# Optimization experiments

Hardware: AMD Instinct MI355X
Metric: run time of the kernel (lower is better)

The kernel has to match this reference:

```python
import jax, jax.numpy as jnp
import numpy as np


def setup_inputs() -> dict:
    key = jax.random.key(0)
    k1, k2 = jax.random.split(key)
    N, M, Q, D = 4096, 128, 64, 128
    a_embeddings = jax.random.normal(k1, (N, D), dtype=jnp.float32)
    b_embedding_sets = jax.random.normal(k2, (M, Q, D), dtype=jnp.float32)
    gaussian_variance = jnp.full((1,), 0.5, dtype=jnp.float32)  # nn.Parameter default
    return {
        "a_embeddings": a_embeddings,
        "b_embedding_sets": b_embedding_sets,
        "gaussian_variance": gaussian_variance,
    }


def reference(a_embeddings, b_embedding_sets, gaussian_variance):
    # Covariance = var * I, so inv(cov) = I / var and the Mahalanobis term is
    # ||a - mu||^2 / var. Expand the squared distance to avoid the NxMxQxD
    # broadcast intermediate the torch code materializes (same math).
    inv_var = 1.0 / gaussian_variance[0]
    a2 = jnp.sum(a_embeddings * a_embeddings, axis=-1)          # [N]
    b2 = jnp.sum(b_embedding_sets * b_embedding_sets, axis=-1)  # [M, Q]
    ab = jnp.einsum("nd,mqd->nmq", a_embeddings, b_embedding_sets)  # [N, M, Q]
    x2 = (a2[:, None, None] - 2.0 * ab + b2[None, :, :]) * inv_var  # [N, M, Q]
    densities = jnp.exp(-0.5 * x2)                  # [N, M, Q]
    dens_per_cluster = densities.sum(axis=2)        # [N, M]
    prob = dens_per_cluster / (dens_per_cluster.sum(axis=1, keepdims=True) + 1e-10)
    return prob
```

## Files before the change

kernel.cpp:

```cpp
#include <hip/hip_runtime.h>
#include <hip/hip_bf16.h>
#include <math.h>

#define NN 4096
#define MM 128
#define QQ 64
#define DD 128
#define CC (MM * QQ)

typedef short bf16x8 __attribute__((ext_vector_type(8)));
typedef float f32x4  __attribute__((ext_vector_type(4)));

static __device__ inline unsigned short f2bf(float f) {
    __hip_bfloat16 h = __float2bfloat16(f);
    return *reinterpret_cast<unsigned short*>(&h);
}

__global__ __launch_bounds__(256)
void prep_kernel(const float* __restrict__ A, const float* __restrict__ B,
                 unsigned short* __restrict__ Abf, unsigned short* __restrict__ Bbf,
                 float* __restrict__ a2, float* __restrict__ b2)
{
    const int row = blockIdx.x * 8 + (threadIdx.x >> 5);
    const int l32 = threadIdx.x & 31;
    const float* src;
    unsigned short* dst;
    float* nrm;
    if (row < NN) { src = A + (size_t)row * DD; dst = Abf + (size_t)row * DD; nrm = a2 + row; }
    else {
        int r = row - NN;
        src = B + (size_t)r * DD; dst = Bbf + (size_t)r * DD; nrm = b2 + r;
    }
    float4 v = ((const float4*)src)[l32];
    ushort4 u;
    u.x = f2bf(v.x); u.y = f2bf(v.y); u.z = f2bf(v.z); u.w = f2bf(v.w);
    ((ushort4*)dst)[l32] = u;
    float s = v.x * v.x + v.y * v.y + v.z * v.z + v.w * v.w;
    #pragma unroll
    for (int m = 16; m > 0; m >>= 1) s += __shfl_xor(s, m, 64);
    if (l32 == 0) *nrm = s;
}

__global__ __launch_bounds__(512, 4)
void kde_mfma_kernel(const unsigned short* __restrict__ Abf,
                     const unsigned short* __restrict__ Bbf,
                     const float* __restrict__ var,
                     const float* __restrict__ a2w,
                     const float* __restrict__ b2w,
                     float* __restrict__ dpc)
{
    __shared__ unsigned short Tile[256 * DD];
    __shared__ float a2s[128];
    __shared__ float b2s[128];
    __shared__ float red[8][32];

    const int lin = blockIdx.x;
    const int xcd = lin & 7;
    const int loc = lin >> 3;
    const int cb  = (xcd << 3) | (loc & 7);
    const int nb  = loc >> 3;
    const int n0  = nb * 128;
    const int c0  = cb * 128;

    const int t    = threadIdx.x;
    const int w    = t >> 6;
    const int lane = t & 63;

    const unsigned short* Ab = Abf + (size_t)n0 * DD;
    const unsigned short* Bb = Bbf + (size_t)c0 * DD;
    #pragma unroll
    for (int i = 0; i < 8; ++i) {
        const int slot = w * 512 + i * 64 + lane;
        const int r    = slot >> 4;
        const int c16  = slot & 15;
        const int scb  = c16 ^ (r & 7);
        const unsigned short* g = (r < 128) ? (Ab + r * DD + scb * 8)
                                            : (Bb + (r - 128) * DD + scb * 8);
        unsigned short* lbase = &Tile[(w * 512 + i * 64) * 8];
        __builtin_amdgcn_global_load_lds(
            (const __attribute__((address_space(1))) unsigned int*)g,
            (__attribute__((address_space(3))) unsigned int*)lbase,
            16, 0, 0);
    }
    if (t < 128)            a2s[t]       = a2w[n0 + t];
    else if (t < 256)       b2s[t - 128] = b2w[c0 + (t - 128)];
    __syncthreads();

    const int l15   = lane & 15;
    const int q     = lane >> 4;
    const int xr    = l15 & 7;
    const int rbase = (w & 3) * 32;
    const int cbase = (w >> 2) * 64;

    f32x4 acc[2][4] = {};
    #pragma unroll
    for (int ks = 0; ks < 4; ++ks) {
        const int off = ((ks * 4 + q) ^ xr) * 8;
        bf16x8 af[2], bf[4];
        #pragma unroll
        for (int i = 0; i < 2; ++i)
            af[i] = *(const bf16x8*)&Tile[(rbase + i * 16 + l15) * DD + off];
        #pragma unroll
        for (int j = 0; j < 4; ++j)
            bf[j] = *(const bf16x8*)&Tile[(128 + cbase + j * 16 + l15) * DD + off];
        #pragma unroll
        for (int i = 0; i < 2; ++i)
            #pragma unroll
            for (int j = 0; j < 4; ++j)
                acc[i][j] = __builtin_amdgcn_mfma_f32_16x16x32_bf16(
                                af[i], bf[j], acc[i][j], 0, 0, 0);
    }

    const float hinv = 0.5f / var[0];
    float rowsum[2][4];
    #pragma unroll
    for (int i = 0; i < 2; ++i) {
        #pragma unroll
        for (int reg = 0; reg < 4; ++reg) {
            const float a2 = a2s[rbase + i * 16 + q * 4 + reg];
            float p = 0.f;
            #pragma unroll
            for (int j = 0; j < 4; ++j) {
                const float b2 = b2s[cbase + j * 16 + l15];
                p += __expf((2.f * acc[i][j][reg] - a2 - b2) * hinv);
            }
            rowsum[i][reg] = p;
        }
    }
    #pragma unroll
    for (int mask = 1; mask < 16; mask <<= 1)
        #pragma unroll
        for (int i = 0; i < 2; ++i)
            #pragma unroll
            for (int reg = 0; reg < 4; ++reg)
                rowsum[i][reg] += __shfl_xor(rowsum[i][reg], mask, 64);

    if (l15 == 0) {
        #pragma unroll
        for (int i = 0; i < 2; ++i)
            #pragma unroll
            for (int reg = 0; reg < 4; ++reg)
                red[w][i * 16 + q * 4 + reg] = rowsum[i][reg];
    }
    const int m = (cb << 1) + (w >> 2);
    if (lane < 32)
        dpc[(size_t)m * NN + n0 + rbase + lane] = red[w][lane];
}

__global__ __launch_bounds__(1024)
void kde_norm_kernel(const float* __restrict__ dpc, float* __restrict__ out)
{
    __shared__ float tile[MM][65];
    __shared__ float rden[64];
    const int n0 = blockIdx.x * 64;
    const int t  = threadIdx.x;

    #pragma unroll
    for (int it = 0; it < 2; ++it) {
        const int m  = (t >> 4) + it * 64;
        const int nc = (t & 15) * 4;
        float4 v = *(const float4*)&dpc[(size_t)m * NN + n0 + nc];
        tile[m][nc]     = v.x;
        tile[m][nc + 1] = v.y;
        tile[m][nc + 2] = v.z;
        tile[m][nc + 3] = v.w;
    }
    __syncthreads();

    if (t < 64) {
        float s = 0.f;
        #pragma unroll 8
        for (int m = 0; m < MM; ++m) s += tile[m][t];
        rden[t] = 1.f / (s + 1e-10f);
    }
    __syncthreads();

    const int nloc = t >> 4;
    const int m0   = (t & 15) * 8;
    const float r  = rden[nloc];
    float4 o0, o1;
    o0.x = tile[m0][nloc] * r;     o0.y = tile[m0 + 1][nloc] * r;
    o0.z = tile[m0 + 2][nloc] * r; o0.w = tile[m0 + 3][nloc] * r;
    o1.x = tile[m0 + 4][nloc] * r; o1.y = tile[m0 + 5][nloc] * r;
    o1.z = tile[m0 + 6][nloc] * r; o1.w = tile[m0 + 7][nloc] * r;
    float* obase = &out[(size_t)(n0 + nloc) * MM + m0];
    *(float4*)obase       = o0;
    *(float4*)(obase + 4) = o1;
}

extern "C" void kernel_launch(void* const* d_in, const int* in_sizes, int n_in,
                              void* d_out, int out_size, void* d_ws, size_t ws_size,
                              hipStream_t stream) {
    const float* A   = (const float*)d_in[0];
    const float* B   = (const float*)d_in[1];
    const float* var = (const float*)d_in[2];
    float* out = (float*)d_out;

    unsigned short* Abf = (unsigned short*)d_ws;
    unsigned short* Bbf = Abf + (size_t)NN * DD;
    float* a2  = (float*)(Bbf + (size_t)CC * DD);
    float* b2  = a2 + NN;
    float* dpc = b2 + CC;

    prep_kernel<<<(NN + CC) / 8, 256, 0, stream>>>(A, B, Abf, Bbf, a2, b2);
    kde_mfma_kernel<<<2048, 512, 0, stream>>>(Abf, Bbf, var, a2, b2, dpc);
    kde_norm_kernel<<<NN / 64, 1024, 0, stream>>>(dpc, out);
}
```

Baseline: 85.90 us.

## Make density kernel persistent over center tiles with double-buffered B loads

Replaces the one-tile-per-block density kernel with 256 blocks that keep a 128-row A tile resident in LDS and iterate over eight 128-center B tiles. The B tiles and their norms are double-buffered via async global-to-LDS loads, so the next tile streams in while the current one is processed. This removes repeated A reloads and per-block launch and setup cost, and stores row sums directly as vectors. The trade-off is lower parallelism: one 8-wave block per CU, with hand-written waitcnt/barrier synchronisation.

```diff
diff --git a/kernel.cpp b/kernel.cpp
--- a/kernel.cpp
+++ b/kernel.cpp
@@ -10,6 +10,9 @@
 
 typedef short bf16x8 __attribute__((ext_vector_type(8)));
 typedef float f32x4  __attribute__((ext_vector_type(4)));
+
+#define AS1 __attribute__((address_space(1)))
+#define AS3 __attribute__((address_space(3)))
 
 static __device__ inline unsigned short f2bf(float f) {
     __hip_bfloat16 h = __float2bfloat16(f);
@@ -41,110 +44,132 @@
     if (l32 == 0) *nrm = s;
 }
 
-__global__ __launch_bounds__(512, 4)
-void kde_mfma_kernel(const unsigned short* __restrict__ Abf,
+__global__ __launch_bounds__(512, 2)
+void kde_dens_kernel(const unsigned short* __restrict__ Abf,
                      const unsigned short* __restrict__ Bbf,
                      const float* __restrict__ var,
                      const float* __restrict__ a2w,
                      const float* __restrict__ b2w,
                      float* __restrict__ dpc)
 {
-    __shared__ unsigned short Tile[256 * DD];
-    __shared__ float a2s[128];
-    __shared__ float b2s[128];
-    __shared__ float red[8][32];
-
-    const int lin = blockIdx.x;
-    const int xcd = lin & 7;
-    const int loc = lin >> 3;
-    const int cb  = (xcd << 3) | (loc & 7);
-    const int nb  = loc >> 3;
-    const int n0  = nb * 128;
-    const int c0  = cb * 128;
-
-    const int t    = threadIdx.x;
-    const int w    = t >> 6;
-    const int lane = t & 63;
-
-    const unsigned short* Ab = Abf + (size_t)n0 * DD;
-    const unsigned short* Bb = Bbf + (size_t)c0 * DD;
-    #pragma unroll
-    for (int i = 0; i < 8; ++i) {
-        const int slot = w * 512 + i * 64 + lane;
-        const int r    = slot >> 4;
-        const int c16  = slot & 15;
-        const int scb  = c16 ^ (r & 7);
-        const unsigned short* g = (r < 128) ? (Ab + r * DD + scb * 8)
-                                            : (Bb + (r - 128) * DD + scb * 8);
-        unsigned short* lbase = &Tile[(w * 512 + i * 64) * 8];
-        __builtin_amdgcn_global_load_lds(
-            (const __attribute__((address_space(1))) unsigned int*)g,
-            (__attribute__((address_space(3))) unsigned int*)lbase,
-            16, 0, 0);
-    }
-    if (t < 128)            a2s[t]       = a2w[n0 + t];
-    else if (t < 256)       b2s[t - 128] = b2w[c0 + (t - 128)];
-    __syncthreads();
-
-    const int l15   = lane & 15;
-    const int q     = lane >> 4;
-    const int xr    = l15 & 7;
-    const int rbase = (w & 3) * 32;
-    const int cbase = (w >> 2) * 64;
-
-    f32x4 acc[2][4] = {};
-    #pragma unroll
-    for (int ks = 0; ks < 4; ++ks) {
-        const int off = ((ks * 4 + q) ^ xr) * 8;
-        bf16x8 af[2], bf[4];
-        #pragma unroll
-        for (int i = 0; i < 2; ++i)
-            af[i] = *(const bf16x8*)&Tile[(rbase + i * 16 + l15) * DD + off];
-        #pragma unroll
-        for (int j = 0; j < 4; ++j)
-            bf[j] = *(const bf16x8*)&Tile[(128 + cbase + j * 16 + l15) * DD + off];
-        #pragma unroll
-        for (int i = 0; i < 2; ++i)
+    __shared__ unsigned short As[128 * DD];
+    __shared__ unsigned short Bs[2][128 * DD];
+    __shared__ float b2s[2][256];
+
+    const int b     = blockIdx.x;
+    const int xcd   = b & 7;
+    const int n0    = (b >> 3) * 128;
+    const int slab0 = xcd * 1024;
+
+    const int t  = threadIdx.x;
+    const int w  = t >> 6, lane = t & 63;
+    const int l15 = lane & 15, q = lane >> 4, xr = l15 & 7;
+    const int rbase = (w >> 1) * 32;
+    const int cbase = (w & 1) * 64;
+
+    float a2v[2][4];
+    #pragma unroll
+    for (int i = 0; i < 2; ++i)
+        #pragma unroll
+        for (int r = 0; r < 4; ++r)
+            a2v[i][r] = a2w[n0 + rbase + i * 16 + q * 4 + r];
+    const float hinv = 0.5f / var[0];
+
+    {
+        const unsigned short* Ab = Abf + (size_t)n0 * DD;
+        #pragma unroll
+        for (int i = 0; i < 4; ++i) {
+            const int slot = w * 256 + i * 64 + lane;
+            const int r = slot >> 4, c16 = slot & 15, scb = c16 ^ (r & 7);
+            __builtin_amdgcn_global_load_lds(
+                (const AS1 unsigned int*)(Ab + r * DD + scb * 8),
+                (AS3 unsigned int*)&As[(w * 256 + i * 64) * 8], 16, 0, 0);
+        }
+    }
+
+    #define ISSUE(ct)                                                              \
+    {                                                                              \
+        const int c0 = slab0 + (ct) * 128;                                         \
+        const unsigned short* Bb = Bbf + (size_t)c0 * DD;                          \
+        unsigned short* Bdst = &Bs[(ct) & 1][0];                                   \
+        _Pragma("unroll")                                                          \
+        for (int i = 0; i < 4; ++i) {                                              \
+            const int slot = w * 256 + i * 64 + lane;                              \
+            const int r = slot >> 4, c16 = slot & 15, scb = c16 ^ (r & 7);         \
+            __builtin_amdgcn_global_load_lds(                                      \
+                (const AS1 unsigned int*)(Bb + r * DD + scb * 8),                  \
+                (AS3 unsigned int*)&Bdst[(w * 256 + i * 64) * 8], 16, 0, 0);       \
+        }                                                                          \
+        __builtin_amdgcn_global_load_lds(                                          \
+            (const AS1 unsigned int*)(b2w + c0 + lane * 4),                        \
+            (AS3 unsigned int*)&b2s[(ct) & 1][0], 16, 0, 0);                       \
+    }
+
+    ISSUE(0);
+    ISSUE(1);
+
+    #pragma unroll
+    for (int ct = 0; ct < 8; ++ct) {
+        asm volatile("s_waitcnt vmcnt(5)" ::: "memory");
+        asm volatile("s_barrier" ::: "memory");
+
+        const unsigned short* Bsc = &Bs[ct & 1][0];
+        const float* b2c = &b2s[ct & 1][0];
+
+        f32x4 acc[2][4] = {};
+        #pragma unroll
+        for (int ks = 0; ks < 4; ++ks) {
+            const int off = ((ks * 4 + q) ^ xr) * 8;
+            bf16x8 af[2], bf[4];
+            #pragma unroll
+            for (int i = 0; i < 2; ++i)
+                af[i] = *(const bf16x8*)&As[(rbase + i * 16 + l15) * DD + off];
             #pragma unroll
             for (int j = 0; j < 4; ++j)
-                acc[i][j] = __builtin_amdgcn_mfma_f32_16x16x32_bf16(
-                                af[i], bf[j], acc[i][j], 0, 0, 0);
-    }
-
-    const float hinv = 0.5f / var[0];
-    float rowsum[2][4];
-    #pragma unroll
-    for (int i = 0; i < 2; ++i) {
-        #pragma unroll
-        for (int reg = 0; reg < 4; ++reg) {
-            const float a2 = a2s[rbase + i * 16 + q * 4 + reg];
-            float p = 0.f;
-            #pragma unroll
-            for (int j = 0; j < 4; ++j) {
-                const float b2 = b2s[cbase + j * 16 + l15];
-                p += __expf((2.f * acc[i][j][reg] - a2 - b2) * hinv);
+                bf[j] = *(const bf16x8*)&Bsc[(cbase + j * 16 + l15) * DD + off];
+            #pragma unroll
+            for (int i = 0; i < 2; ++i)
+                #pragma unroll
+                for (int j = 0; j < 4; ++j)
+                    acc[i][j] = __builtin_amdgcn_mfma_f32_16x16x32_bf16(
+                                    af[i], bf[j], acc[i][j], 0, 0, 0);
+        }
+
+        float rowsum[2][4];
+        #pragma unroll
+        for (int i = 0; i < 2; ++i) {
+            #pragma unroll
+            for (int reg = 0; reg < 4; ++reg) {
+                float p = 0.f;
+                #pragma unroll
+                for (int j = 0; j < 4; ++j) {
+                    const float b2 = b2c[cbase + j * 16 + l15];
+                    p += __expf((2.f * acc[i][j][reg] - a2v[i][reg] - b2) * hinv);
+                }
+                rowsum[i][reg] = p;
             }
-            rowsum[i][reg] = p;
-        }
-    }
-    #pragma unroll
-    for (int mask = 1; mask < 16; mask <<= 1)
-        #pragma unroll
-        for (int i = 0; i < 2; ++i)
-            #pragma unroll
-            for (int reg = 0; reg < 4; ++reg)
-                rowsum[i][reg] += __shfl_xor(rowsum[i][reg], mask, 64);
-
-    if (l15 == 0) {
-        #pragma unroll
-        for (int i = 0; i < 2; ++i)
-            #pragma unroll
-            for (int reg = 0; reg < 4; ++reg)
-                red[w][i * 16 + q * 4 + reg] = rowsum[i][reg];
-    }
-    const int m = (cb << 1) + (w >> 2);
-    if (lane < 32)
-        dpc[(size_t)m * NN + n0 + rbase + lane] = red[w][lane];
+        }
+        #pragma unroll
+        for (int mask = 1; mask < 16; mask <<= 1)
+            #pragma unroll
+            for (int i = 0; i < 2; ++i)
+                #pragma unroll
+                for (int reg = 0; reg < 4; ++reg)
+                    rowsum[i][reg] += __shfl_xor(rowsum[i][reg], mask, 64);
+
+        if (l15 == 0) {
+            const int m = xcd * 16 + ct * 2 + (w & 1);
+            #pragma unroll
+            for (int i = 0; i < 2; ++i) {
+                f32x4 o = {rowsum[i][0], rowsum[i][1], rowsum[i][2], rowsum[i][3]};
+                *(f32x4*)&dpc[(size_t)m * NN + n0 + rbase + i * 16 + q * 4] = o;
+            }
+        }
+
+        asm volatile("s_barrier" ::: "memory");
+        if (ct < 6) ISSUE(ct + 2);
+    }
+    #undef ISSUE
 }
 
 __global__ __launch_bounds__(1024)
@@ -203,6 +228,6 @@
     float* dpc = b2 + CC;
 
     prep_kernel<<<(NN + CC) / 8, 256, 0, stream>>>(A, B, Abf, Bbf, a2, b2);
-    kde_mfma_kernel<<<2048, 512, 0, stream>>>(Abf, Bbf, var, a2, b2, dpc);
+    kde_dens_kernel<<<256, 512, 0, stream>>>(Abf, Bbf, var, a2, b2, dpc);
     kde_norm_kernel<<<NN / 64, 1024, 0, stream>>>(dpc, out);
 }
```

Result: no change. 87.13 us (+1.4%).
